# Kernel optimization log

Measured on AMD Instinct MI355X. Metric: run time of the kernel, lower is better.

Reference implementation:

```python
import jax, jax.numpy as jnp
import numpy as np

TEMPERATURE = 1.0  # nn.Parameter(requires_grad=False) -> constant


def setup_inputs() -> dict:
    key = jax.random.key(0)
    k1, k2 = jax.random.split(key)
    B, T, H = 4, 4096, 256
    h_seq = jax.random.normal(k1, (B, T, H), dtype=jnp.float32)
    t = jax.random.uniform(k2, (B, T, 1), dtype=jnp.float32)
    return {"h_seq": h_seq, "t": t}


def reference(h_seq, t):
    # h_seq: [B,T,H], t: [B,T,1]
    T = h_seq.shape[1]
    tau = max(TEMPERATURE, 1e-6)  # temperature.clamp_min(1e-6)
    tq = t[:, :, None, 0]  # [B,T,1]
    tk = t[:, None, :, 0]  # [B,1,T]
    delta = tq - tk  # [B,T,T]
    logits = -jnp.square(T * delta) / (tau * tau)  # [B,T,T]
    w = jax.nn.softmax(logits, axis=-1)  # [B,T,T]
    return jnp.einsum('bkj,bjh->bkh', w, h_seq)  # [B,T,H]
```

## Files before the change

kernel.cpp:

```cpp
#include <hip/hip_runtime.h>
#include <hip/hip_bf16.h>


constexpr int Bb = 4;
constexpr int Tt = 4096;
constexpr int Hh = 256;
constexpr int NB = 1024;

__global__ __launch_bounds__(1024) void sort_kernel(
    const float* __restrict__ tvals,
    float* __restrict__ sorted_t,
    int* __restrict__ sorted_idx,
    int* __restrict__ offsets)
{
    __shared__ int hist[NB];
    __shared__ int excl[NB];
    __shared__ int cnt[NB];
    __shared__ int wsum[16];
    __shared__ int wexcl[16];

    const int b   = blockIdx.x;
    const int tid = threadIdx.x;
    const int lane = tid & 63;
    const int wv   = tid >> 6;
    const float* tb = tvals + (size_t)b * Tt;

    hist[tid] = 0;
    cnt[tid]  = 0;
    __syncthreads();

    float tv[4]; int bk[4];
    #pragma unroll
    for (int i = 0; i < 4; ++i) {
        const int j = i * 1024 + tid;
        const float t = tb[j];
        int k = (int)(t * (float)NB);
        k = k < 0 ? 0 : (k > NB - 1 ? NB - 1 : k);
        tv[i] = t; bk[i] = k;
        atomicAdd(&hist[k], 1);
    }
    __syncthreads();

    const int self = hist[tid];
    int x = self;
    #pragma unroll
    for (int d = 1; d < 64; d <<= 1) {
        const int y = __shfl_up(x, d);
        if (lane >= d) x += y;
    }
    if (lane == 63) wsum[wv] = x;
    __syncthreads();
    if (tid < 16) {
        int y = wsum[tid];
        #pragma unroll
        for (int d = 1; d < 16; d <<= 1) {
            const int z = __shfl_up(y, d);
            if (tid >= d) y += z;
        }
        wexcl[tid] = y - wsum[tid];
    }
    __syncthreads();
    const int incl = x + wexcl[wv];
    excl[tid] = incl - self;
    offsets[(size_t)b * (NB + 1) + tid] = incl - self;
    if (tid == 0) offsets[(size_t)b * (NB + 1) + NB] = Tt;
    __syncthreads();

    #pragma unroll
    for (int i = 0; i < 4; ++i) {
        const int k = bk[i];
        const int rank = atomicAdd(&cnt[k], 1);
        const int pos = excl[k] + rank;
        sorted_t[(size_t)b * Tt + pos]   = tv[i];
        sorted_idx[(size_t)b * Tt + pos] = i * 1024 + tid;
    }
}

constexpr int QPW = 4;
constexpr int MTHREADS = 256;

__global__ __launch_bounds__(MTHREADS) void stattn_sparse(
    const float* __restrict__ h_seq,
    const float* __restrict__ sorted_t,
    const int* __restrict__ sorted_idx,
    const int* __restrict__ offsets,
    float* __restrict__ out)
{
    const int tid  = threadIdx.x;
    const int lane = tid & 63;
    const int wv   = tid >> 6;

    const int phys = blockIdx.x;
    const int lb   = (phys & 7) * 128 + (phys >> 3);
    const int b    = lb >> 8;
    const int blk  = lb & 255;

    const float* st = sorted_t  + (size_t)b * Tt;
    const int*   si = sorted_idx + (size_t)b * Tt;
    const int*   off = offsets + (size_t)b * (NB + 1);
    const float* hb = h_seq + (size_t)b * Tt * Hh;
    const float Tf = (float)Tt;

    const int p0 = blk * 16 + wv * QPW;

    float tq[QPW]; int qi[QPW];
    #pragma unroll
    for (int g = 0; g < QPW; ++g) { tq[g] = st[p0 + g]; qi[g] = si[p0 + g]; }

    int bmin = (int)(tq[0] * (float)NB);
    int bmax = (int)(tq[QPW - 1] * (float)NB);
    bmin = bmin < 0 ? 0 : (bmin > NB - 1 ? NB - 1 : bmin);
    bmax = bmax < 0 ? 0 : (bmax > NB - 1 ? NB - 1 : bmax);
    const int blo = bmin - 2 < 0 ? 0 : bmin - 2;
    const int bhi = bmax + 3 > NB ? NB : bmax + 3;
    const int lo = off[blo];
    const int hi = off[bhi];

    float4 acc[QPW];
    float  den[QPW];
    #pragma unroll
    for (int g = 0; g < QPW; ++g) {
        acc[g] = make_float4(0.f, 0.f, 0.f, 0.f);
        den[g] = 0.f;
    }

    for (int base = lo; base < hi; base += 64) {
        const int p = base + lane;
        const bool valid = p < hi;
        const float tj = valid ? st[p] : 1e9f;
        const int   jj = valid ? si[p] : 0;

        float w[QPW]; float wmax = 0.f;
        #pragma unroll
        for (int g = 0; g < QPW; ++g) {
            const float x = Tf * (tq[g] - tj);
            w[g] = __expf(-x * x);
            den[g] += w[g];
            wmax = fmaxf(wmax, w[g]);
        }

        unsigned long long mask = __ballot(wmax > 1e-20f);
        while (mask) {
            const int s0 = __builtin_ctzll(mask); mask &= mask - 1;
            const bool has2 = mask != 0;
            const int s1 = has2 ? __builtin_ctzll(mask) : s0;
            if (has2) mask &= mask - 1;

            const int j0 = __shfl(jj, s0);
            const int j1 = __shfl(jj, s1);
            const float4 h0 = *(const float4*)&hb[(size_t)j0 * Hh + lane * 4];
            const float4 h1 = *(const float4*)&hb[(size_t)j1 * Hh + lane * 4];

            #pragma unroll
            for (int g = 0; g < QPW; ++g) {
                const float a0 = __shfl(w[g], s0);
                float a1 = __shfl(w[g], s1);
                if (!has2) a1 = 0.f;
                acc[g].x += a0 * h0.x; acc[g].x += a1 * h1.x;
                acc[g].y += a0 * h0.y; acc[g].y += a1 * h1.y;
                acc[g].z += a0 * h0.z; acc[g].z += a1 * h1.z;
                acc[g].w += a0 * h0.w; acc[g].w += a1 * h1.w;
            }
        }
    }

    #pragma unroll
    for (int g = 0; g < QPW; ++g) {
        float d = den[g];
        #pragma unroll
        for (int s = 1; s < 64; s <<= 1) d += __shfl_xor(d, s);
        den[g] = d;
    }

    #pragma unroll
    for (int g = 0; g < QPW; ++g) {
        const float inv = 1.0f / den[g];
        float* orow = out + ((size_t)b * Tt + qi[g]) * Hh + lane * 4;
        float4 o;
        o.x = acc[g].x * inv; o.y = acc[g].y * inv;
        o.z = acc[g].z * inv; o.w = acc[g].w * inv;
        *(float4*)orow = o;
    }
}

constexpr int QB = 64;
constexpr int JB = 64;
constexpr int NT = Tt / JB;
constexpr int NTHREADS = 512;

__device__ __forceinline__ void gld16(const void* g, void* l) {
    __builtin_amdgcn_global_load_lds(
        (const __attribute__((address_space(1))) void*)g,
        (__attribute__((address_space(3))) void*)l, 16, 0, 0);
}
__device__ __forceinline__ void gld4(const void* g, void* l) {
    __builtin_amdgcn_global_load_lds(
        (const __attribute__((address_space(1))) void*)g,
        (__attribute__((address_space(3))) void*)l, 4, 0, 0);
}

__global__ __launch_bounds__(NTHREADS, 2) void stattn_kernel(
    const float* __restrict__ h_seq,
    const float* __restrict__ tvals,
    float* __restrict__ out)
{
    __shared__ float hbuf[2][JB][Hh];
    __shared__ float wbuf[JB][QB];
    __shared__ float tjbuf[2][JB];
    __shared__ float sden[QB];
    __shared__ float tqs[QB];

    const int tid  = threadIdx.x;
    const int lane = tid & 63;
    const int wv   = tid >> 6;
    const int phys = blockIdx.x;
    const int lb   = (phys & 7) * 32 + (phys >> 3);
    const int b    = lb >> 6;
    const int qt   = lb & 63;
    const int q0   = qt * QB;

    const float* hb = h_seq + (size_t)b * Tt * Hh;
    const float* tb = tvals + (size_t)b * Tt;

    if (tid < QB) { tqs[tid] = tb[q0 + tid]; sden[tid] = 0.0f; }

    float acc[8][4];
    #pragma unroll
    for (int k = 0; k < 8; ++k)
        #pragma unroll
        for (int c = 0; c < 4; ++c) acc[k][c] = 0.0f;

    const float Tf = (float)Tt;

    auto stage = [&](int buf, int tile) {
        const float* src = hb + (size_t)tile * JB * Hh;
        float* dst = &hbuf[buf][0][0];
        #pragma unroll
        for (int i = 0; i < 8; ++i) {
            const int off = i * (NTHREADS * 4) + tid * 4;
            gld16(src + off, dst + off);
        }
        gld4(tb + tile * JB + lane, &tjbuf[buf][lane]);
    };

    stage(0, 0);
    __syncthreads();

    const int qw = wv * 8;

    for (int t = 0; t < NT; ++t) {
        const int cur = t & 1;
        __syncthreads();
        {
            const int q  = tid & 63;
            const int jg = tid >> 6;
            const float tq = tqs[q];
            const float4 tj0 = *(const float4*)&tjbuf[cur][jg * 8];
            const float4 tj1 = *(const float4*)&tjbuf[cur][jg * 8 + 4];
            const float tjv[8] = {tj0.x, tj0.y, tj0.z, tj0.w,
                                  tj1.x, tj1.y, tj1.z, tj1.w};
            float part = 0.0f;
            #pragma unroll
            for (int jj = 0; jj < 8; ++jj) {
                const float d = Tf * (tq - tjv[jj]);
                const float w = __expf(-d * d);
                wbuf[jg * 8 + jj][q] = w;
                part += w;
            }
            atomicAdd(&sden[q], part);
        }
        if (t + 1 < NT) stage((t + 1) & 1, t + 1);
        asm volatile("s_waitcnt lgkmcnt(0)" ::: "memory");
        __builtin_amdgcn_s_barrier();
        asm volatile("" ::: "memory");
        #pragma unroll 2
        for (int j = 0; j < JB; ++j) {
            const float4 hv = *(const float4*)&hbuf[cur][j][lane * 4];
            const float4 w0 = *(const float4*)&wbuf[j][qw];
            const float4 w1 = *(const float4*)&wbuf[j][qw + 4];
            const float wr[8] = {w0.x, w0.y, w0.z, w0.w,
                                 w1.x, w1.y, w1.z, w1.w};
            #pragma unroll
            for (int k = 0; k < 8; ++k) {
                acc[k][0] += wr[k] * hv.x;
                acc[k][1] += wr[k] * hv.y;
                acc[k][2] += wr[k] * hv.z;
                acc[k][3] += wr[k] * hv.w;
            }
        }
    }

    #pragma unroll
    for (int k = 0; k < 8; ++k) {
        const int q = q0 + qw + k;
        const float inv = 1.0f / sden[qw + k];
        float4 o;
        o.x = acc[k][0] * inv;
        o.y = acc[k][1] * inv;
        o.z = acc[k][2] * inv;
        o.w = acc[k][3] * inv;
        *(float4*)&out[((size_t)b * Tt + q) * Hh + (size_t)(lane * 4)] = o;
    }
}

extern "C" void kernel_launch(void* const* d_in, const int* in_sizes, int n_in,
                              void* d_out, int out_size, void* d_ws, size_t ws_size,
                              hipStream_t stream) {
    const float* h_seq = (const float*)d_in[0];
    const float* tvals = (const float*)d_in[1];
    float* out = (float*)d_out;

    const size_t need = (size_t)Bb * Tt * 4 * 2 + (size_t)Bb * (NB + 1) * 4;
    if (ws_size >= need) {
        float* sorted_t   = (float*)d_ws;
        int*   sorted_idx = (int*)(sorted_t + (size_t)Bb * Tt);
        int*   offsets    = (int*)(sorted_idx + (size_t)Bb * Tt);
        sort_kernel<<<dim3(Bb), dim3(1024), 0, stream>>>(
            tvals, sorted_t, sorted_idx, offsets);
        stattn_sparse<<<dim3(Bb * (Tt / 16)), dim3(MTHREADS), 0, stream>>>(
            h_seq, sorted_t, sorted_idx, offsets, out);
    } else {
        stattn_kernel<<<dim3(Bb * (Tt / QB)), dim3(NTHREADS), 0, stream>>>(
            h_seq, tvals, out);
    }
}
```

Baseline: 23.61 us.

## Pack sorted keys, pre-scale times, double queries per wave, gather four rows per step

The sort kernel now writes interleaved (scaled time, index) pairs, with times pre-multiplied by T, so the attention kernel reads one 8-byte load per key and skips a multiply. Each wave now handles 8 queries instead of 4, so every gathered h row is reused across more queries, and the grid is halved. The inner gather loop consumes four active keys per iteration instead of two, which exposes more memory-level parallelism. In exchange it uses more registers, which may lower occupancy, and the key window per wave gets wider, so more keys are visited.

```diff
diff --git a/kernel.cpp b/kernel.cpp
--- a/kernel.cpp
+++ b/kernel.cpp
@@ -9,8 +9,7 @@
 
 __global__ __launch_bounds__(1024) void sort_kernel(
     const float* __restrict__ tvals,
-    float* __restrict__ sorted_t,
-    int* __restrict__ sorted_idx,
+    uint2* __restrict__ spair,
     int* __restrict__ offsets)
 {
     __shared__ int hist[NB];
@@ -19,8 +18,8 @@
     __shared__ int wsum[16];
     __shared__ int wexcl[16];
 
-    const int b   = blockIdx.x;
-    const int tid = threadIdx.x;
+    const int b    = blockIdx.x;
+    const int tid  = threadIdx.x;
     const int lane = tid & 63;
     const int wv   = tid >> 6;
     const float* tb = tvals + (size_t)b * Tt;
@@ -36,7 +35,8 @@
         const float t = tb[j];
         int k = (int)(t * (float)NB);
         k = k < 0 ? 0 : (k > NB - 1 ? NB - 1 : k);
-        tv[i] = t; bk[i] = k;
+        tv[i] = t * 4096.0f;
+        bk[i] = k;
         atomicAdd(&hist[k], 1);
     }
     __syncthreads();
@@ -71,18 +71,19 @@
         const int k = bk[i];
         const int rank = atomicAdd(&cnt[k], 1);
         const int pos = excl[k] + rank;
-        sorted_t[(size_t)b * Tt + pos]   = tv[i];
-        sorted_idx[(size_t)b * Tt + pos] = i * 1024 + tid;
-    }
-}
-
-constexpr int QPW = 4;
+        uint2 pr;
+        pr.x = __float_as_uint(tv[i]);
+        pr.y = (unsigned)(i * 1024 + tid);
+        spair[(size_t)b * Tt + pos] = pr;
+    }
+}
+
+constexpr int QPW = 8;
 constexpr int MTHREADS = 256;
 
 __global__ __launch_bounds__(MTHREADS) void stattn_sparse(
     const float* __restrict__ h_seq,
-    const float* __restrict__ sorted_t,
-    const int* __restrict__ sorted_idx,
+    const uint2* __restrict__ spair,
     const int* __restrict__ offsets,
     float* __restrict__ out)
 {
@@ -91,24 +92,26 @@
     const int wv   = tid >> 6;
 
     const int phys = blockIdx.x;
-    const int lb   = (phys & 7) * 128 + (phys >> 3);
-    const int b    = lb >> 8;
-    const int blk  = lb & 255;
-
-    const float* st = sorted_t  + (size_t)b * Tt;
-    const int*   si = sorted_idx + (size_t)b * Tt;
+    const int lb   = (phys & 7) * 64 + (phys >> 3);
+    const int b    = lb >> 7;
+    const int blk  = lb & 127;
+
+    const uint2* sp  = spair + (size_t)b * Tt;
     const int*   off = offsets + (size_t)b * (NB + 1);
-    const float* hb = h_seq + (size_t)b * Tt * Hh;
-    const float Tf = (float)Tt;
-
-    const int p0 = blk * 16 + wv * QPW;
+    const float* hb  = h_seq + (size_t)b * Tt * Hh;
+
+    const int p0 = blk * 32 + wv * QPW;
 
     float tq[QPW]; int qi[QPW];
     #pragma unroll
-    for (int g = 0; g < QPW; ++g) { tq[g] = st[p0 + g]; qi[g] = si[p0 + g]; }
-
-    int bmin = (int)(tq[0] * (float)NB);
-    int bmax = (int)(tq[QPW - 1] * (float)NB);
+    for (int g = 0; g < QPW; ++g) {
+        const uint2 pr = sp[p0 + g];
+        tq[g] = __uint_as_float(pr.x);
+        qi[g] = (int)pr.y;
+    }
+
+    int bmin = (int)(tq[0] * 0.25f);
+    int bmax = (int)(tq[QPW - 1] * 0.25f);
     bmin = bmin < 0 ? 0 : (bmin > NB - 1 ? NB - 1 : bmin);
     bmax = bmax < 0 ? 0 : (bmax > NB - 1 ? NB - 1 : bmax);
     const int blo = bmin - 2 < 0 ? 0 : bmin - 2;
@@ -127,13 +130,14 @@
     for (int base = lo; base < hi; base += 64) {
         const int p = base + lane;
         const bool valid = p < hi;
-        const float tj = valid ? st[p] : 1e9f;
-        const int   jj = valid ? si[p] : 0;
+        float tj; int jj;
+        if (valid) { const uint2 pr = sp[p]; tj = __uint_as_float(pr.x); jj = (int)pr.y; }
+        else       { tj = 3.0e18f; jj = 0; }
 
         float w[QPW]; float wmax = 0.f;
         #pragma unroll
         for (int g = 0; g < QPW; ++g) {
-            const float x = Tf * (tq[g] - tj);
+            const float x = tq[g] - tj;
             w[g] = __expf(-x * x);
             den[g] += w[g];
             wmax = fmaxf(wmax, w[g]);
@@ -142,24 +146,39 @@
         unsigned long long mask = __ballot(wmax > 1e-20f);
         while (mask) {
             const int s0 = __builtin_ctzll(mask); mask &= mask - 1;
-            const bool has2 = mask != 0;
-            const int s1 = has2 ? __builtin_ctzll(mask) : s0;
-            if (has2) mask &= mask - 1;
+            const bool h1 = mask != 0;
+            const int s1 = h1 ? __builtin_ctzll(mask) : s0; if (h1) mask &= mask - 1;
+            const bool h2 = mask != 0;
+            const int s2 = h2 ? __builtin_ctzll(mask) : s0; if (h2) mask &= mask - 1;
+            const bool h3 = mask != 0;
+            const int s3 = h3 ? __builtin_ctzll(mask) : s0; if (h3) mask &= mask - 1;
 
             const int j0 = __shfl(jj, s0);
             const int j1 = __shfl(jj, s1);
-            const float4 h0 = *(const float4*)&hb[(size_t)j0 * Hh + lane * 4];
-            const float4 h1 = *(const float4*)&hb[(size_t)j1 * Hh + lane * 4];
+            const int j2 = __shfl(jj, s2);
+            const int j3 = __shfl(jj, s3);
+            float4 h0 = *(const float4*)&hb[(size_t)j0 * Hh + lane * 4];
+            float4 h1v = *(const float4*)&hb[(size_t)j1 * Hh + lane * 4];
+            float4 h2v = *(const float4*)&hb[(size_t)j2 * Hh + lane * 4];
+            float4 h3v = *(const float4*)&hb[(size_t)j3 * Hh + lane * 4];
+            if (!h1) { h1v.x = 0.f; h1v.y = 0.f; h1v.z = 0.f; h1v.w = 0.f; }
+            if (!h2) { h2v.x = 0.f; h2v.y = 0.f; h2v.z = 0.f; h2v.w = 0.f; }
+            if (!h3) { h3v.x = 0.f; h3v.y = 0.f; h3v.z = 0.f; h3v.w = 0.f; }
 
             #pragma unroll
             for (int g = 0; g < QPW; ++g) {
                 const float a0 = __shfl(w[g], s0);
-                float a1 = __shfl(w[g], s1);
-                if (!has2) a1 = 0.f;
-                acc[g].x += a0 * h0.x; acc[g].x += a1 * h1.x;
-                acc[g].y += a0 * h0.y; acc[g].y += a1 * h1.y;
-                acc[g].z += a0 * h0.z; acc[g].z += a1 * h1.z;
-                acc[g].w += a0 * h0.w; acc[g].w += a1 * h1.w;
+                const float a1 = __shfl(w[g], s1);
+                const float a2 = __shfl(w[g], s2);
+                const float a3 = __shfl(w[g], s3);
+                acc[g].x += a0 * h0.x; acc[g].y += a0 * h0.y;
+                acc[g].z += a0 * h0.z; acc[g].w += a0 * h0.w;
+                acc[g].x += a1 * h1v.x; acc[g].y += a1 * h1v.y;
+                acc[g].z += a1 * h1v.z; acc[g].w += a1 * h1v.w;
+                acc[g].x += a2 * h2v.x; acc[g].y += a2 * h2v.y;
+                acc[g].z += a2 * h2v.z; acc[g].w += a2 * h2v.w;
+                acc[g].x += a3 * h3v.x; acc[g].y += a3 * h3v.y;
+                acc[g].z += a3 * h3v.z; acc[g].w += a3 * h3v.w;
             }
         }
     }
@@ -254,7 +273,7 @@
         {
             const int q  = tid & 63;
             const int jg = tid >> 6;
-            const float tq = tqs[q];
+            const float tqv = tqs[q];
             const float4 tj0 = *(const float4*)&tjbuf[cur][jg * 8];
             const float4 tj1 = *(const float4*)&tjbuf[cur][jg * 8 + 4];
             const float tjv[8] = {tj0.x, tj0.y, tj0.z, tj0.w,
@@ -262,7 +281,7 @@
             float part = 0.0f;
             #pragma unroll
             for (int jj = 0; jj < 8; ++jj) {
-                const float d = Tf * (tq - tjv[jj]);
+                const float d = Tf * (tqv - tjv[jj]);
                 const float w = __expf(-d * d);
                 wbuf[jg * 8 + jj][q] = w;
                 part += w;
@@ -310,15 +329,13 @@
     const float* tvals = (const float*)d_in[1];
     float* out = (float*)d_out;
 
-    const size_t need = (size_t)Bb * Tt * 4 * 2 + (size_t)Bb * (NB + 1) * 4;
+    const size_t need = (size_t)Bb * Tt * sizeof(uint2) + (size_t)Bb * (NB + 1) * 4;
     if (ws_size >= need) {
-        float* sorted_t   = (float*)d_ws;
-        int*   sorted_idx = (int*)(sorted_t + (size_t)Bb * Tt);
-        int*   offsets    = (int*)(sorted_idx + (size_t)Bb * Tt);
-        sort_kernel<<<dim3(Bb), dim3(1024), 0, stream>>>(
-            tvals, sorted_t, sorted_idx, offsets);
-        stattn_sparse<<<dim3(Bb * (Tt / 16)), dim3(MTHREADS), 0, stream>>>(
-            h_seq, sorted_t, sorted_idx, offsets, out);
+        uint2* spair  = (uint2*)d_ws;
+        int*   offsets = (int*)(spair + (size_t)Bb * Tt);
+        sort_kernel<<<dim3(Bb), dim3(1024), 0, stream>>>(tvals, spair, offsets);
+        stattn_sparse<<<dim3(Bb * (Tt / 32)), dim3(MTHREADS), 0, stream>>>(
+            h_seq, spair, offsets, out);
     } else {
         stattn_kernel<<<dim3(Bb * (Tt / QB)), dim3(NTHREADS), 0, stream>>>(
             h_seq, tvals, out);
```

After: 22.62 us (median of 3 runs). 1.04x faster.
